# Kernel optimization log

Measured on AMD Instinct MI355X. Metric: run time of the kernel, lower is better.

## Reference

```python
import jax, jax.numpy as jnp
import numpy as np

N = 50000
E = 800000
D_IN = 256
HID = 256
EPS = 1e-12


def _glorot(key, shape):
    fan_in, fan_out = shape[1], shape[0]
    lim = jnp.sqrt(6.0 / (fan_in + fan_out))
    return jax.random.uniform(key, shape, jnp.float32, -lim, lim)


def setup_inputs() -> dict:
    key = jax.random.key(0)
    ks = jax.random.split(key, 8)
    x = jax.random.normal(ks[0], (N, D_IN), jnp.float32)
    edge_index = jax.random.randint(ks[1], (2, E), 0, N, jnp.int64)
    # SAGEConv params: lin_l (neighbor, with bias), lin_r (root, no bias)
    W1l = _glorot(ks[2], (HID, D_IN))
    b1l = jnp.zeros((HID,), jnp.float32)
    W1r = _glorot(ks[3], (HID, D_IN))
    W2l = _glorot(ks[4], (HID, HID))
    b2l = jnp.zeros((HID,), jnp.float32)
    W2r = _glorot(ks[5], (HID, HID))
    return {"x": x, "edge_index": edge_index,
            "W1l": W1l, "b1l": b1l, "W1r": W1r,
            "W2l": W2l, "b2l": b2l, "W2r": W2r}


def _sage_conv(x, src, dst, Wl, bl, Wr, num_nodes):
    # mean aggregation of source features onto destination nodes
    agg = jax.ops.segment_sum(x[src], dst, num_segments=num_nodes)          # [N, d]
    cnt = jax.ops.segment_sum(jnp.ones((src.shape[0],), x.dtype), dst,
                              num_segments=num_nodes)                        # [N]
    mean = agg / jnp.maximum(cnt, 1.0)[:, None]
    out = mean @ Wl.T + bl + x @ Wr.T                                        # [N, out]
    # L2 normalize (normalize=True)
    norm = jnp.linalg.norm(out, axis=-1, keepdims=True)
    return out / jnp.maximum(norm, EPS)


def reference(x, edge_index, W1l, b1l, W1r, W2l, b2l, W2r):
    src, dst = edge_index[0], edge_index[1]
    n = x.shape[0]
    h = _sage_conv(x, src, dst, W1l, b1l, W1r, n)
    h = jax.nn.relu(h)
    h = _sage_conv(h, src, dst, W2l, b2l, W2r, n)
    return h
```

## Files before the change

### kernel.cpp

```cpp
#include <hip/hip_runtime.h>
#include <hip/hip_bf16.h>


#define DD 256
#define NPB 128
#define CSRCAP 2048

typedef unsigned short ushort_t;
using bf16x8 = __attribute__((ext_vector_type(8))) short;
using f32x4  = __attribute__((ext_vector_type(4))) float;
using i32x4  = __attribute__((ext_vector_type(4))) int;

static __device__ __forceinline__ float b2f(ushort_t u) {
    __hip_bfloat16 h = *reinterpret_cast<__hip_bfloat16*>(&u);
    return __bfloat162float(h);
}
static __device__ __forceinline__ ushort_t f2b(float f) {
    __hip_bfloat16 h = __float2bfloat16(f);
    return *reinterpret_cast<ushort_t*>(&h);
}

static __device__ __forceinline__ void load16(const ushort_t* g, ushort_t* l) {
    __builtin_amdgcn_global_load_lds(
        (const __attribute__((address_space(1))) unsigned*)(g),
        (__attribute__((address_space(3))) unsigned*)(l),
        16, 0, 0);
}

static __device__ __forceinline__ size_t sma(int npad, int node, int col) {
    return ((size_t)(col >> 5) * npad + node) * 32 + (col & 31);
}


__global__ __launch_bounds__(256) void prep_kernel(
        const int* __restrict__ ei, int* __restrict__ bcnt, int E, int eb2,
        const float* __restrict__ x, ushort_t* __restrict__ xb, int xe, int cxb,
        int npad,
        const float* __restrict__ w1l, const float* __restrict__ w1r,
        const float* __restrict__ w2l, const float* __restrict__ w2r,
        ushort_t* __restrict__ wc1, ushort_t* __restrict__ wc2) {
    int b = blockIdx.x;
    int tid = threadIdx.x;
    if (b < eb2) {
        __shared__ int hist[512];
        for (int i = tid; i < 512; i += 256) hist[i] = 0;
        __syncthreads();
        #pragma unroll
        for (int j = 0; j < 8; j++) {
            int e = b * 2048 + j * 256 + tid;
            if (e < E) atomicAdd(&hist[ei[E + e] >> 7], 1);
        }
        __syncthreads();
        for (int i = tid; i < 512; i += 256) {
            int h = hist[i];
            if (h) atomicAdd(&bcnt[i], h);
        }
        return;
    }
    b -= eb2;
    if (b < cxb) {
        int i = (b * 256 + tid) * 8;
        if (i + 8 > xe) return;
        int node = i >> 8, col = i & 255;
        float4 a = *(const float4*)(x + i);
        float4 c = *(const float4*)(x + i + 4);
        ushort_t o[8] = {f2b(a.x), f2b(a.y), f2b(a.z), f2b(a.w),
                         f2b(c.x), f2b(c.y), f2b(c.z), f2b(c.w)};
        *(i32x4*)(xb + sma(npad, node, col)) = *(const i32x4*)o;
        return;
    }
    b -= cxb;
    {
        int i = (b * 256 + tid) * 8;
        int which = i >> 16;
        int o = i & 65535;
        int row = o >> 8, col = o & 255;
        const float* src = (which == 0) ? w1l : (which == 1) ? w1r
                          : (which == 2) ? w2l : w2r;
        ushort_t* dst = ((which < 2) ? wc1 : wc2)
                        + (size_t)row * 512 + (which & 1) * 256 + col;
        float4 a = *(const float4*)(src + o);
        float4 c = *(const float4*)(src + o + 4);
        ushort_t ov[8] = {f2b(a.x), f2b(a.y), f2b(a.z), f2b(a.w),
                          f2b(c.x), f2b(c.y), f2b(c.z), f2b(c.w)};
        *(i32x4*)dst = *(const i32x4*)ov;
    }
}


__global__ __launch_bounds__(512) void bucket_scan_kernel(
        const int* __restrict__ bcnt, int* __restrict__ bbase,
        int* __restrict__ bcur, int* __restrict__ offs,
        int nbuck, int N, int E) {
    __shared__ int wt[8];
    int tid = threadIdx.x;
    int wave = tid >> 6, lane = tid & 63;
    int c = (tid < nbuck) ? bcnt[tid] : 0;
    int incl = c;
    #pragma unroll
    for (int off = 1; off < 64; off <<= 1) {
        int t = __shfl_up(incl, off);
        if (lane >= off) incl += t;
    }
    if (lane == 63) wt[wave] = incl;
    __syncthreads();
    int woff = 0;
    for (int w = 0; w < wave; w++) woff += wt[w];
    int excl = woff + incl - c;
    if (tid < nbuck) { bbase[tid] = excl; bcur[tid] = excl; }
    if (tid == 0) offs[N] = E;
}


__global__ __launch_bounds__(256) void part_kernel(const int* __restrict__ ei,
                                                   int* __restrict__ bcur,
                                                   int2* __restrict__ stage,
                                                   int E, int nbuck) {
    __shared__ int hist[512];
    __shared__ int gbase[512];
    int tid = threadIdx.x;
    for (int i = tid; i < nbuck; i += 256) hist[i] = 0;
    __syncthreads();
    int sv[8], dv[8], bk[8], rk[8];
    #pragma unroll
    for (int j = 0; j < 8; j++) {
        int e = blockIdx.x * 2048 + j * 256 + tid;
        if (e < E) {
            sv[j] = ei[e];
            dv[j] = ei[E + e];
            bk[j] = dv[j] / NPB;
            rk[j] = atomicAdd(&hist[bk[j]], 1);
        } else bk[j] = -1;
    }
    __syncthreads();
    for (int i = tid; i < nbuck; i += 256) {
        int h = hist[i];
        gbase[i] = h ? atomicAdd(&bcur[i], h) : 0;
    }
    __syncthreads();
    #pragma unroll
    for (int j = 0; j < 8; j++)
        if (bk[j] >= 0) {
            int p = gbase[bk[j]] + rk[j];
            stage[p] = make_int2(sv[j], dv[j]);
        }
}

__global__ __launch_bounds__(256) void group_kernel(const int2* __restrict__ stage,
                                                    const int* __restrict__ bbase,
                                                    const int* __restrict__ bcnt,
                                                    int* __restrict__ offs,
                                                    int* __restrict__ csr, int N) {
    __shared__ int ldeg[NPB];
    __shared__ int lpos[NPB];
    __shared__ int wsum;
    int b = blockIdx.x;
    int lo = b * NPB;
    int gcnt = min(N - lo, NPB);
    int tid = threadIdx.x;
    if (tid < NPB) ldeg[tid] = 0;
    __syncthreads();
    int base = bbase[b];
    int m = bcnt[b];
    for (int t = tid; t < m; t += 256)
        atomicAdd(&ldeg[stage[base + t].y - lo], 1);
    __syncthreads();
    int v = (tid < NPB) ? ldeg[tid] : 0;
    int incl = v;
    #pragma unroll
    for (int off = 1; off < 64; off <<= 1) {
        int t = __shfl_up(incl, off);
        if ((tid & 63) >= off) incl += t;
    }
    if (tid == 63) wsum = incl;
    __syncthreads();
    int excl = incl - v + ((tid >= 64 && tid < NPB) ? wsum : 0);
    if (tid < NPB) lpos[tid] = base + excl;
    if (tid < gcnt) offs[lo + tid] = base + excl;
    __syncthreads();
    for (int t = tid; t < m; t += 256) {
        int2 e = stage[base + t];
        int p = atomicAdd(&lpos[e.y - lo], 1);
        csr[p] = e.x;
    }
}


static __device__ __forceinline__ void add8(float* acc, i32x4 v) {
    const unsigned* u = (const unsigned*)&v;
    #pragma unroll
    for (int j = 0; j < 4; j++) {
        acc[2 * j]     += __uint_as_float(u[j] << 16);
        acc[2 * j + 1] += __uint_as_float(u[j] & 0xffff0000u);
    }
}

__global__ __launch_bounds__(256) void agg_kernel(const ushort_t* __restrict__ F,
                                                  const int* __restrict__ csr,
                                                  const int* __restrict__ offs,
                                                  ushort_t* __restrict__ mean,
                                                  int N, int npad) {
    __shared__ int lidx[CSRCAP];
    __shared__ int soffs[65];
    int s = blockIdx.x & 7;
    int g0 = (blockIdx.x >> 3) * 64;
    int tid = threadIdx.x;
    int gcnt = min(N - g0, 64);
    if (tid <= gcnt) soffs[tid] = offs[g0 + tid];
    __syncthreads();
    int base = soffs[0];
    int total = soffs[gcnt] - base;
    int stg = min(total, CSRCAP);
    for (int i = tid; i < stg; i += 256) lidx[i] = csr[base + i];
    __syncthreads();

    int node = tid >> 2, ch = tid & 3;
    if (node >= gcnt) return;
    const ushort_t* Fs = F + ((size_t)s * npad) * 32 + ch * 8;
    int beg = soffs[node] - base, end = soffs[node + 1] - base;

    float acc[8];
    #pragma unroll
    for (int j = 0; j < 8; j++) acc[j] = 0.f;

    if (total <= CSRCAP) {
        int i = beg;
        for (; i + 4 <= end; i += 4) {
            i32x4 v0 = *(const i32x4*)(Fs + (size_t)lidx[i]     * 32);
            i32x4 v1 = *(const i32x4*)(Fs + (size_t)lidx[i + 1] * 32);
            i32x4 v2 = *(const i32x4*)(Fs + (size_t)lidx[i + 2] * 32);
            i32x4 v3 = *(const i32x4*)(Fs + (size_t)lidx[i + 3] * 32);
            add8(acc, v0); add8(acc, v1); add8(acc, v2); add8(acc, v3);
        }
        for (; i < end; i++) {
            i32x4 v = *(const i32x4*)(Fs + (size_t)lidx[i] * 32);
            add8(acc, v);
        }
    } else {
        for (int i = beg; i < end; i++) {
            i32x4 v = *(const i32x4*)(Fs + (size_t)csr[base + i] * 32);
            add8(acc, v);
        }
    }

    float scale = 1.f / fmaxf((float)(end - beg), 1.f);
    ushort_t o[8];
    #pragma unroll
    for (int j = 0; j < 8; j++) o[j] = f2b(acc[j] * scale);
    *(i32x4*)(mean + ((size_t)s * npad + g0 + node) * 32 + ch * 8) = *(const i32x4*)o;
}


__global__ __launch_bounds__(512, 4) void gemm_norm_kernel(
        const ushort_t* __restrict__ meanb,
        const ushort_t* __restrict__ fb,
        const ushort_t* __restrict__ W,
        const float*    __restrict__ bias,
        ushort_t* __restrict__ outb,
        float*    __restrict__ outf,
        int npad, int N, int relu) {
    __shared__ union {
        struct {
            ushort_t As[128 * 64];
            ushort_t Bs[256 * 64];
        } s;
        ushort_t ebuf[64 * 264];
    } u;
    __shared__ float rowsq[128];

    int tid = threadIdx.x;
    int wave = tid >> 6, lane = tid & 63;
    int quad = lane >> 4, m16 = lane & 15;
    int swz = m16 & 7;
    int rowhalf = wave >> 2;
    int colq = wave & 3;
    int rowbase = blockIdx.x * 128;

    if (tid < 128) rowsq[tid] = 0.f;

    f32x4 acc[4][4];
    #pragma unroll
    for (int i = 0; i < 4; i++)
        #pragma unroll
        for (int j = 0; j < 4; j++)
            acc[i][j] = (f32x4){0.f, 0.f, 0.f, 0.f};

    for (int ki = 0; ki < 8; ki++) {
        int kb = ki * 64;
        const ushort_t* Ab = (ki < 4) ? meanb : fb;
        int kl = kb & 255;
        __syncthreads();
        #pragma unroll
        for (int t = 0; t < 2; t++) {
            int instr = wave * 2 + t;
            int flat = instr * 64 + lane;
            int row = flat >> 3, cc = flat & 7;
            int ccg = cc ^ (row & 7);
            int c = kl + ccg * 8;
            load16(Ab + sma(npad, rowbase + row, c), &u.s.As[instr * 512]);
        }
        #pragma unroll
        for (int t = 0; t < 4; t++) {
            int instr = wave * 4 + t;
            int flat = instr * 64 + lane;
            int row = flat >> 3, cc = flat & 7;
            int ccg = cc ^ (row & 7);
            load16(W + (size_t)row * 512 + kb + ccg * 8, &u.s.Bs[instr * 512]);
        }
        __syncthreads();

        #pragma unroll
        for (int ks = 0; ks < 2; ks++) {
            int cbase = ks * 4 + quad;
            bf16x8 af[4], bfr[4];
            #pragma unroll
            for (int rt = 0; rt < 4; rt++) {
                int r = rowhalf * 64 + rt * 16 + m16;
                af[rt] = *(const bf16x8*)&u.s.As[r * 64 + ((cbase ^ swz)) * 8];
            }
            #pragma unroll
            for (int ct = 0; ct < 4; ct++) {
                int r = colq * 64 + ct * 16 + m16;
                bfr[ct] = *(const bf16x8*)&u.s.Bs[r * 64 + ((cbase ^ swz)) * 8];
            }
            #pragma unroll
            for (int rt = 0; rt < 4; rt++)
                #pragma unroll
                for (int ct = 0; ct < 4; ct++)
                    acc[rt][ct] = __builtin_amdgcn_mfma_f32_16x16x32_bf16(
                        af[rt], bfr[ct], acc[rt][ct], 0, 0, 0);
        }
    }

    float bvals[4];
    #pragma unroll
    for (int ct = 0; ct < 4; ct++)
        bvals[ct] = bias[colq * 64 + ct * 16 + m16];
    #pragma unroll
    for (int rt = 0; rt < 4; rt++) {
        #pragma unroll
        for (int reg = 0; reg < 4; reg++) {
            float s = 0.f;
            #pragma unroll
            for (int ct = 0; ct < 4; ct++) {
                float v = acc[rt][ct][reg] + bvals[ct];
                acc[rt][ct][reg] = v;
                s += v * v;
            }
            #pragma unroll
            for (int off = 1; off < 16; off <<= 1)
                s += __shfl_xor(s, off);
            if (m16 == 0)
                atomicAdd(&rowsq[rowhalf * 64 + rt * 16 + quad * 4 + reg], s);
        }
    }
    __syncthreads();

    #pragma unroll
    for (int p = 0; p < 2; p++) {
        if (rowhalf == p) {
            #pragma unroll
            for (int rt = 0; rt < 4; rt++) {
                #pragma unroll
                for (int reg = 0; reg < 4; reg++) {
                    int rl = rt * 16 + quad * 4 + reg;
                    float inv = 1.f / fmaxf(sqrtf(rowsq[p * 64 + rl]), 1e-12f);
                    #pragma unroll
                    for (int ct = 0; ct < 4; ct++) {
                        float v = acc[rt][ct][reg] * inv;
                        if (relu) v = fmaxf(v, 0.f);
                        int col = colq * 64 + ct * 16 + m16;
                        u.ebuf[rl * 264 + col] = f2b(v);
                    }
                }
            }
        }
        __syncthreads();
        #pragma unroll
        for (int j = 0; j < 4; j++) {
            int flat = j * 512 + tid;
            int row = flat >> 5, cc = flat & 31;
            int gr = rowbase + p * 64 + row;
            if (gr < N) {
                bf16x8 v = *(const bf16x8*)&u.ebuf[row * 264 + cc * 8];
                if (outf) {
                    float4 f0, f1;
                    f0.x = b2f((ushort_t)v[0]); f0.y = b2f((ushort_t)v[1]);
                    f0.z = b2f((ushort_t)v[2]); f0.w = b2f((ushort_t)v[3]);
                    f1.x = b2f((ushort_t)v[4]); f1.y = b2f((ushort_t)v[5]);
                    f1.z = b2f((ushort_t)v[6]); f1.w = b2f((ushort_t)v[7]);
                    float* ptr = outf + (size_t)gr * 256 + cc * 8;
                    *(float4*)ptr = f0;
                    *(float4*)(ptr + 4) = f1;
                } else {
                    *(bf16x8*)(outb + sma(npad, gr, cc * 8)) = v;
                }
            }
        }
        __syncthreads();
    }
}


static inline size_t align_up(size_t x, size_t a) { return (x + a - 1) & ~(a - 1); }

extern "C" void kernel_launch(void* const* d_in, const int* in_sizes, int n_in,
                              void* d_out, int out_size, void* d_ws, size_t ws_size,
                              hipStream_t stream) {
    const float* x   = (const float*)d_in[0];
    const int*   ei  = (const int*)d_in[1];
    const float* W1l = (const float*)d_in[2];
    const float* b1l = (const float*)d_in[3];
    const float* W1r = (const float*)d_in[4];
    const float* W2l = (const float*)d_in[5];
    const float* b2l = (const float*)d_in[6];
    const float* W2r = (const float*)d_in[7];

    int N = in_sizes[0] / DD;
    int E = in_sizes[1] / 2;
    int npad = N + 128;
    int nbuck = (N + NPB - 1) / NPB;

    char* ws = (char*)d_ws;
    size_t off = 0;
    int* bcnt = (int*)(ws + off);     off = align_up(off + (size_t)512 * 4, 256);
    int* bbase = (int*)(ws + off);    off = align_up(off + (size_t)512 * 4, 256);
    int* bcur = (int*)(ws + off);     off = align_up(off + (size_t)512 * 4, 256);
    int* offs = (int*)(ws + off);     off = align_up(off + (size_t)(N + 1) * 4, 256);
    int* csr = (int*)(ws + off);      off = align_up(off + (size_t)E * 4, 256);
    size_t sstage = off;
    int2* stage = (int2*)(ws + sstage);
    size_t meansz = (size_t)npad * 32 * 8 * 2;
    off = align_up(sstage + ((size_t)E * 8 > meansz ? (size_t)E * 8 : meansz), 256);
    ushort_t* meanb = (ushort_t*)(ws + sstage);
    ushort_t* xb = (ushort_t*)(ws + off);  off = align_up(off + meansz, 256);
    ushort_t* hb = (ushort_t*)(ws + off);  off = align_up(off + meansz, 256);
    ushort_t* wc1 = (ushort_t*)(ws + off); off = align_up(off + (size_t)256 * 512 * 2, 256);
    ushort_t* wc2 = (ushort_t*)(ws + off); off = align_up(off + (size_t)256 * 512 * 2, 256);

    hipMemsetAsync(bcnt, 0, (size_t)512 * 4, stream);

    int xe = N * DD;
    int eb2 = (E + 2047) / 2048;
    int cxb = (xe / 8 + 255) / 256;
    int cwb = (4 * DD * DD / 8) / 256;
    prep_kernel<<<eb2 + cxb + cwb, 256, 0, stream>>>(ei, bcnt, E, eb2,
                                                     x, xb, xe, cxb, npad,
                                                     W1l, W1r, W2l, W2r, wc1, wc2);

    bucket_scan_kernel<<<1, 512, 0, stream>>>(bcnt, bbase, bcur, offs, nbuck, N, E);

    int pb = (E + 2047) / 2048;
    part_kernel<<<pb, 256, 0, stream>>>(ei, bcur, stage, E, nbuck);
    group_kernel<<<nbuck, 256, 0, stream>>>(stage, bbase, bcnt, offs, csr, N);

    int ab = 8 * ((N + 63) / 64);
    int gb = (N + 127) / 128;

    agg_kernel<<<ab, 256, 0, stream>>>(xb, csr, offs, meanb, N, npad);
    gemm_norm_kernel<<<gb, 512, 0, stream>>>(meanb, xb, wc1, b1l,
                                             hb, (float*)nullptr, npad, N, 1);

    agg_kernel<<<ab, 256, 0, stream>>>(hb, csr, offs, meanb, N, npad);
    gemm_norm_kernel<<<gb, 512, 0, stream>>>(meanb, hb, wc2, b2l,
                                             (ushort_t*)nullptr, (float*)d_out, npad, N, 0);
}
```

Measured before the change: 279.2 us.

## Halve GEMM row tile to 64 and unroll neighbor gather by eight

The fused GEMM+L2-norm kernel now handles 64 rows per block instead of 128. That doubles the grid (about 782 blocks), cuts the accumulator registers per wave in half, and lets the epilogue write everything in one pass. The aim is better occupancy and load balance across CUs, but each block reloads the full 256x512 weight tile for half as many rows, so weight traffic through LDS per output row doubles. The aggregation kernel also unrolls its CSR gather loop from 4 to 8 and hoists the index loads, putting more loads in flight.

New measurement: 289.3 us. 1.04x slower.

```diff
diff --git a/kernel.cpp b/kernel.cpp
--- a/kernel.cpp
+++ b/kernel.cpp
@@ -225,12 +225,21 @@
 
     if (total <= CSRCAP) {
         int i = beg;
-        for (; i + 4 <= end; i += 4) {
-            i32x4 v0 = *(const i32x4*)(Fs + (size_t)lidx[i]     * 32);
-            i32x4 v1 = *(const i32x4*)(Fs + (size_t)lidx[i + 1] * 32);
-            i32x4 v2 = *(const i32x4*)(Fs + (size_t)lidx[i + 2] * 32);
-            i32x4 v3 = *(const i32x4*)(Fs + (size_t)lidx[i + 3] * 32);
+        for (; i + 8 <= end; i += 8) {
+            int x0 = lidx[i],     x1 = lidx[i + 1];
+            int x2 = lidx[i + 2], x3 = lidx[i + 3];
+            int x4 = lidx[i + 4], x5 = lidx[i + 5];
+            int x6 = lidx[i + 6], x7 = lidx[i + 7];
+            i32x4 v0 = *(const i32x4*)(Fs + (size_t)x0 * 32);
+            i32x4 v1 = *(const i32x4*)(Fs + (size_t)x1 * 32);
+            i32x4 v2 = *(const i32x4*)(Fs + (size_t)x2 * 32);
+            i32x4 v3 = *(const i32x4*)(Fs + (size_t)x3 * 32);
+            i32x4 v4 = *(const i32x4*)(Fs + (size_t)x4 * 32);
+            i32x4 v5 = *(const i32x4*)(Fs + (size_t)x5 * 32);
+            i32x4 v6 = *(const i32x4*)(Fs + (size_t)x6 * 32);
+            i32x4 v7 = *(const i32x4*)(Fs + (size_t)x7 * 32);
             add8(acc, v0); add8(acc, v1); add8(acc, v2); add8(acc, v3);
+            add8(acc, v4); add8(acc, v5); add8(acc, v6); add8(acc, v7);
         }
         for (; i < end; i++) {
             i32x4 v = *(const i32x4*)(Fs + (size_t)lidx[i] * 32);
@@ -261,12 +270,12 @@
         int npad, int N, int relu) {
     __shared__ union {
         struct {
-            ushort_t As[128 * 64];
+            ushort_t As[64 * 64];
             ushort_t Bs[256 * 64];
         } s;
         ushort_t ebuf[64 * 264];
     } u;
-    __shared__ float rowsq[128];
+    __shared__ float rowsq[64];
 
     int tid = threadIdx.x;
     int wave = tid >> 6, lane = tid & 63;
@@ -274,13 +283,13 @@
     int swz = m16 & 7;
     int rowhalf = wave >> 2;
     int colq = wave & 3;
-    int rowbase = blockIdx.x * 128;
-
-    if (tid < 128) rowsq[tid] = 0.f;
-
-    f32x4 acc[4][4];
-    #pragma unroll
-    for (int i = 0; i < 4; i++)
+    int rowbase = blockIdx.x * 64;
+
+    if (tid < 64) rowsq[tid] = 0.f;
+
+    f32x4 acc[2][4];
+    #pragma unroll
+    for (int i = 0; i < 2; i++)
         #pragma unroll
         for (int j = 0; j < 4; j++)
             acc[i][j] = (f32x4){0.f, 0.f, 0.f, 0.f};
@@ -290,14 +299,10 @@
         const ushort_t* Ab = (ki < 4) ? meanb : fb;
         int kl = kb & 255;
         __syncthreads();
-        #pragma unroll
-        for (int t = 0; t < 2; t++) {
-            int instr = wave * 2 + t;
-            int flat = instr * 64 + lane;
-            int row = flat >> 3, cc = flat & 7;
+        {
+            int row = tid >> 3, cc = tid & 7;
             int ccg = cc ^ (row & 7);
-            int c = kl + ccg * 8;
-            load16(Ab + sma(npad, rowbase + row, c), &u.s.As[instr * 512]);
+            load16(Ab + sma(npad, rowbase + row, kl + ccg * 8), &u.s.As[wave * 512]);
         }
         #pragma unroll
         for (int t = 0; t < 4; t++) {
@@ -312,19 +317,20 @@
         #pragma unroll
         for (int ks = 0; ks < 2; ks++) {
             int cbase = ks * 4 + quad;
-            bf16x8 af[4], bfr[4];
-            #pragma unroll
-            for (int rt = 0; rt < 4; rt++) {
-                int r = rowhalf * 64 + rt * 16 + m16;
-                af[rt] = *(const bf16x8*)&u.s.As[r * 64 + ((cbase ^ swz)) * 8];
+            int pc = (cbase ^ swz) * 8;
+            bf16x8 af[2], bfr[4];
+            #pragma unroll
+            for (int rt = 0; rt < 2; rt++) {
+                int r = rowhalf * 32 + rt * 16 + m16;
+                af[rt] = *(const bf16x8*)&u.s.As[r * 64 + pc];
             }
             #pragma unroll
             for (int ct = 0; ct < 4; ct++) {
                 int r = colq * 64 + ct * 16 + m16;
-                bfr[ct] = *(const bf16x8*)&u.s.Bs[r * 64 + ((cbase ^ swz)) * 8];
+                bfr[ct] = *(const bf16x8*)&u.s.Bs[r * 64 + pc];
             }
             #pragma unroll
-            for (int rt = 0; rt < 4; rt++)
+            for (int rt = 0; rt < 2; rt++)
                 #pragma unroll
                 for (int ct = 0; ct < 4; ct++)
                     acc[rt][ct] = __builtin_amdgcn_mfma_f32_16x16x32_bf16(
@@ -337,7 +343,7 @@
     for (int ct = 0; ct < 4; ct++)
         bvals[ct] = bias[colq * 64 + ct * 16 + m16];
     #pragma unroll
-    for (int rt = 0; rt < 4; rt++) {
+    for (int rt = 0; rt < 2; rt++) {
         #pragma unroll
         for (int reg = 0; reg < 4; reg++) {
             float s = 0.f;
@@ -351,53 +357,47 @@
             for (int off = 1; off < 16; off <<= 1)
                 s += __shfl_xor(s, off);
             if (m16 == 0)
-                atomicAdd(&rowsq[rowhalf * 64 + rt * 16 + quad * 4 + reg], s);
-        }
-    }
-    __syncthreads();
-
-    #pragma unroll
-    for (int p = 0; p < 2; p++) {
-        if (rowhalf == p) {
-            #pragma unroll
-            for (int rt = 0; rt < 4; rt++) {
-                #pragma unroll
-                for (int reg = 0; reg < 4; reg++) {
-                    int rl = rt * 16 + quad * 4 + reg;
-                    float inv = 1.f / fmaxf(sqrtf(rowsq[p * 64 + rl]), 1e-12f);
-                    #pragma unroll
-                    for (int ct = 0; ct < 4; ct++) {
-                        float v = acc[rt][ct][reg] * inv;
-                        if (relu) v = fmaxf(v, 0.f);
-                        int col = colq * 64 + ct * 16 + m16;
-                        u.ebuf[rl * 264 + col] = f2b(v);
-                    }
-                }
+                atomicAdd(&rowsq[rowhalf * 32 + rt * 16 + quad * 4 + reg], s);
+        }
+    }
+    __syncthreads();
+
+    #pragma unroll
+    for (int rt = 0; rt < 2; rt++) {
+        #pragma unroll
+        for (int reg = 0; reg < 4; reg++) {
+            int rl = rowhalf * 32 + rt * 16 + quad * 4 + reg;
+            float inv = 1.f / fmaxf(sqrtf(rowsq[rl]), 1e-12f);
+            #pragma unroll
+            for (int ct = 0; ct < 4; ct++) {
+                float v = acc[rt][ct][reg] * inv;
+                if (relu) v = fmaxf(v, 0.f);
+                int col = colq * 64 + ct * 16 + m16;
+                u.ebuf[rl * 264 + col] = f2b(v);
             }
         }
-        __syncthreads();
-        #pragma unroll
-        for (int j = 0; j < 4; j++) {
-            int flat = j * 512 + tid;
-            int row = flat >> 5, cc = flat & 31;
-            int gr = rowbase + p * 64 + row;
-            if (gr < N) {
-                bf16x8 v = *(const bf16x8*)&u.ebuf[row * 264 + cc * 8];
-                if (outf) {
-                    float4 f0, f1;
-                    f0.x = b2f((ushort_t)v[0]); f0.y = b2f((ushort_t)v[1]);
-                    f0.z = b2f((ushort_t)v[2]); f0.w = b2f((ushort_t)v[3]);
-                    f1.x = b2f((ushort_t)v[4]); f1.y = b2f((ushort_t)v[5]);
-                    f1.z = b2f((ushort_t)v[6]); f1.w = b2f((ushort_t)v[7]);
-                    float* ptr = outf + (size_t)gr * 256 + cc * 8;
-                    *(float4*)ptr = f0;
-                    *(float4*)(ptr + 4) = f1;
-                } else {
-                    *(bf16x8*)(outb + sma(npad, gr, cc * 8)) = v;
-                }
+    }
+    __syncthreads();
+    #pragma unroll
+    for (int j = 0; j < 4; j++) {
+        int flat = j * 512 + tid;
+        int row = flat >> 5, cc = flat & 31;
+        int gr = rowbase + row;
+        if (gr < N) {
+            bf16x8 v = *(const bf16x8*)&u.ebuf[row * 264 + cc * 8];
+            if (outf) {
+                float4 f0, f1;
+                f0.x = b2f((ushort_t)v[0]); f0.y = b2f((ushort_t)v[1]);
+                f0.z = b2f((ushort_t)v[2]); f0.w = b2f((ushort_t)v[3]);
+                f1.x = b2f((ushort_t)v[4]); f1.y = b2f((ushort_t)v[5]);
+                f1.z = b2f((ushort_t)v[6]); f1.w = b2f((ushort_t)v[7]);
+                float* ptr = outf + (size_t)gr * 256 + cc * 8;
+                *(float4*)ptr = f0;
+                *(float4*)(ptr + 4) = f1;
+            } else {
+                *(bf16x8*)(outb + sma(npad, gr, cc * 8)) = v;
             }
         }
-        __syncthreads();
     }
 }
 
@@ -455,7 +455,7 @@
     group_kernel<<<nbuck, 256, 0, stream>>>(stage, bbase, bcnt, offs, csr, N);
 
     int ab = 8 * ((N + 63) / 64);
-    int gb = (N + 127) / 128;
+    int gb = (N + 63) / 64;
 
     agg_kernel<<<ab, 256, 0, stream>>>(xb, csr, offs, meanb, N, npad);
     gemm_norm_kernel<<<gb, 512, 0, stream>>>(meanb, xb, wc1, b1l,
```

## Load GEMM MFMA operands directly from global memory instead of LDS staging

Applied to the files above, without the earlier changes.

The GEMM kernel stops staging A and W tiles into shared memory through global_load_lds with barriers. Each wave now reads its MFMA fragments straight from global memory using the sliced layout, with the k-loop fully unrolled. This removes two barriers per k-step and the LDS traffic, and it shrinks LDS use to the epilogue buffer, which may allow more resident blocks. The cost is that operand reuse across waves moves from LDS to L1/L2, so each W row and A row is fetched several times per block, and load latency is no longer hidden by any explicit staging.

Result: slower. 327.4 us (+17.3%).

```diff
diff --git a/kernel.cpp b/kernel.cpp
--- a/kernel.cpp
+++ b/kernel.cpp
@@ -18,13 +18,6 @@
 static __device__ __forceinline__ ushort_t f2b(float f) {
     __hip_bfloat16 h = __float2bfloat16(f);
     return *reinterpret_cast<ushort_t*>(&h);
-}
-
-static __device__ __forceinline__ void load16(const ushort_t* g, ushort_t* l) {
-    __builtin_amdgcn_global_load_lds(
-        (const __attribute__((address_space(1))) unsigned*)(g),
-        (__attribute__((address_space(3))) unsigned*)(l),
-        16, 0, 0);
 }
 
 static __device__ __forceinline__ size_t sma(int npad, int node, int col) {
@@ -259,19 +252,12 @@
         ushort_t* __restrict__ outb,
         float*    __restrict__ outf,
         int npad, int N, int relu) {
-    __shared__ union {
-        struct {
-            ushort_t As[128 * 64];
-            ushort_t Bs[256 * 64];
-        } s;
-        ushort_t ebuf[64 * 264];
-    } u;
+    __shared__ ushort_t ebuf[64 * 264];
     __shared__ float rowsq[128];
 
     int tid = threadIdx.x;
     int wave = tid >> 6, lane = tid & 63;
     int quad = lane >> 4, m16 = lane & 15;
-    int swz = m16 & 7;
     int rowhalf = wave >> 2;
     int colq = wave & 3;
     int rowbase = blockIdx.x * 128;
@@ -285,44 +271,30 @@
         for (int j = 0; j < 4; j++)
             acc[i][j] = (f32x4){0.f, 0.f, 0.f, 0.f};
 
+    size_t aoff[4];
+    #pragma unroll
+    for (int rt = 0; rt < 4; rt++)
+        aoff[rt] = (size_t)(rowbase + rowhalf * 64 + rt * 16 + m16) * 32 + quad * 8;
+    const ushort_t* wrow[4];
+    #pragma unroll
+    for (int ct = 0; ct < 4; ct++)
+        wrow[ct] = W + (size_t)(colq * 64 + ct * 16 + m16) * 512 + quad * 8;
+
+    #pragma unroll
     for (int ki = 0; ki < 8; ki++) {
         int kb = ki * 64;
         const ushort_t* Ab = (ki < 4) ? meanb : fb;
-        int kl = kb & 255;
-        __syncthreads();
-        #pragma unroll
-        for (int t = 0; t < 2; t++) {
-            int instr = wave * 2 + t;
-            int flat = instr * 64 + lane;
-            int row = flat >> 3, cc = flat & 7;
-            int ccg = cc ^ (row & 7);
-            int c = kl + ccg * 8;
-            load16(Ab + sma(npad, rowbase + row, c), &u.s.As[instr * 512]);
-        }
-        #pragma unroll
-        for (int t = 0; t < 4; t++) {
-            int instr = wave * 4 + t;
-            int flat = instr * 64 + lane;
-            int row = flat >> 3, cc = flat & 7;
-            int ccg = cc ^ (row & 7);
-            load16(W + (size_t)row * 512 + kb + ccg * 8, &u.s.Bs[instr * 512]);
-        }
-        __syncthreads();
-
+        int sl0 = (kb & 255) >> 5;
         #pragma unroll
         for (int ks = 0; ks < 2; ks++) {
-            int cbase = ks * 4 + quad;
+            const ushort_t* As = Ab + (size_t)(sl0 + ks) * npad * 32;
             bf16x8 af[4], bfr[4];
             #pragma unroll
-            for (int rt = 0; rt < 4; rt++) {
-                int r = rowhalf * 64 + rt * 16 + m16;
-                af[rt] = *(const bf16x8*)&u.s.As[r * 64 + ((cbase ^ swz)) * 8];
-            }
-            #pragma unroll
-            for (int ct = 0; ct < 4; ct++) {
-                int r = colq * 64 + ct * 16 + m16;
-                bfr[ct] = *(const bf16x8*)&u.s.Bs[r * 64 + ((cbase ^ swz)) * 8];
-            }
+            for (int rt = 0; rt < 4; rt++)
+                af[rt] = *(const bf16x8*)(As + aoff[rt]);
+            #pragma unroll
+            for (int ct = 0; ct < 4; ct++)
+                bfr[ct] = *(const bf16x8*)(wrow[ct] + kb + ks * 32);
             #pragma unroll
             for (int rt = 0; rt < 4; rt++)
                 #pragma unroll
@@ -331,6 +303,8 @@
                         af[rt], bfr[ct], acc[rt][ct], 0, 0, 0);
         }
     }
+
+    __syncthreads();
 
     float bvals[4];
     #pragma unroll
@@ -370,7 +344,7 @@
                         float v = acc[rt][ct][reg] * inv;
                         if (relu) v = fmaxf(v, 0.f);
                         int col = colq * 64 + ct * 16 + m16;
-                        u.ebuf[rl * 264 + col] = f2b(v);
+                        ebuf[rl * 264 + col] = f2b(v);
                     }
                 }
             }
@@ -382,7 +356,7 @@
             int row = flat >> 5, cc = flat & 31;
             int gr = rowbase + p * 64 + row;
             if (gr < N) {
-                bf16x8 v = *(const bf16x8*)&u.ebuf[row * 264 + cc * 8];
+                bf16x8 v = *(const bf16x8*)&ebuf[row * 264 + cc * 8];
                 if (outf) {
                     float4 f0, f1;
                     f0.x = b2f((ushort_t)v[0]); f0.y = b2f((ushort_t)v[1]);
```
